# Kernel tuning notes

Hardware: AMD Instinct MI355X
Metric: run time of the kernel (lower is better)

The kernel has to match this reference:

```python
import jax, jax.numpy as jnp
import numpy as np

N_CODES = 1024
DIM = 64
COMMITMENT = 0.25


def setup_inputs() -> dict:
    key = jax.random.key(0)
    k1, k2 = jax.random.split(key)
    z = jax.random.normal(k1, (32, DIM, 64, 64), dtype=jnp.float32)
    # nn.Embedding weight initialized uniform(-1/n_codes, 1/n_codes)
    codebook = jax.random.uniform(
        k2, (N_CODES, DIM), dtype=jnp.float32,
        minval=-1.0 / N_CODES, maxval=1.0 / N_CODES)
    return {"z": z, "codebook": codebook}


def reference(z, codebook):
    B, C, H, W = z.shape
    # (B,C,H,W) -> (B*H*W, C)
    z_flat = jnp.transpose(z, (0, 2, 3, 1)).reshape(-1, C)
    # squared L2 distances via expansion: |z|^2 + |e|^2 - 2 z.e
    dists = (
        jnp.sum(z_flat ** 2, axis=1, keepdims=True)
        + jnp.sum(codebook ** 2, axis=1)
        - 2.0 * z_flat @ codebook.T
    )  # [N, n_codes]
    indices = jnp.argmin(dists, axis=1)  # [N]
    z_q = jnp.transpose(codebook[indices].reshape(B, H, W, C), (0, 3, 1, 2))
    commit_loss = jnp.mean((jax.lax.stop_gradient(z_q) - z) ** 2)
    codebook_loss = jnp.mean((z_q - jax.lax.stop_gradient(z)) ** 2)
    vq_loss = codebook_loss + COMMITMENT * commit_loss
    z_q_st = z + jax.lax.stop_gradient(z_q - z)  # straight-through
    return (z_q_st, vq_loss)
```

## Files before the change

### kernel.cpp

```cpp
#include <hip/hip_runtime.h>


constexpr int DIM    = 64;
constexpr int NCODES = 1024;
constexpr int HWSZ   = 4096;
constexpr int NPOS   = 131072;
constexpr int BLOCK  = 1024;
constexpr int PPB    = 512;
constexpr int GRID   = NPOS / PPB;
constexpr int CIP    = 68;

typedef float    f32x4  __attribute__((ext_vector_type(4)));
typedef int      int4v  __attribute__((ext_vector_type(4)));
typedef unsigned uint4v __attribute__((ext_vector_type(4)));

__global__ __launch_bounds__(BLOCK, 4) void vq_all(const float* __restrict__ z,
                                                   const float* __restrict__ cb,
                                                   float* __restrict__ out) {
    __shared__ __align__(16) unsigned char cb_lds[NCODES * DIM];
    __shared__ int   cinit_lds[16 * CIP];
    __shared__ int   bj_lds[PPB];
    __shared__ float ls_lds[BLOCK / 64];

    const int tid  = threadIdx.x;
    const int w    = tid >> 6;
    const int lane = tid & 63;
    const int q    = lane >> 4;
    const int r    = lane & 15;
    const int p0   = blockIdx.x * PPB;
    const int b    = p0 >> 12;
    const int hwb  = p0 & 4095;

    {
        const int j = tid;
        const float4* src = (const float4*)(cb + (size_t)j * DIM);
        unsigned words[16];
        int nq = 0;
#pragma unroll
        for (int w4 = 0; w4 < 16; w4++) {
            float4 v = src[w4];
            int i0 = __float2int_rn(v.x * 65536.f);
            int i1 = __float2int_rn(v.y * 65536.f);
            int i2 = __float2int_rn(v.z * 65536.f);
            int i3 = __float2int_rn(v.w * 65536.f);
            nq += i0 * i0 + i1 * i1 + i2 * i2 + i3 * i3;
            words[w4] = (unsigned)((i0 & 255) | ((i1 & 255) << 8)
                                 | ((i2 & 255) << 16) | (i3 << 24));
        }
        const int Cj = 262144 - ((nq + 4096) >> 13);
        const int sswz = (j & 3) ^ ((j >> 2) & 1);
#pragma unroll
        for (int u = 0; u < 4; u++) {
            int us = u ^ sswz;
            uint4v tq = {words[4 * u], words[4 * u + 1],
                         words[4 * u + 2], words[4 * u + 3]};
            *(uint4v*)&cb_lds[(size_t)j * 64 + us * 16] = tq;
        }
        cinit_lds[(j & 15) * CIP + (j >> 4)] = (Cj << 10) + (1023 - j);
    }

    int4v afragI[2];
    float zsq[2];
#pragma unroll
    for (int s = 0; s < 2; s++) {
        const float* zb = z + (size_t)b * DIM * HWSZ + hwb + s * 256 + w * 16 + r;
        float sq = 0.f;
        unsigned dw[4];
#pragma unroll
        for (int d = 0; d < 4; d++) {
            float v0 = zb[(size_t)(q * 16 + 4 * d + 0) * HWSZ];
            float v1 = zb[(size_t)(q * 16 + 4 * d + 1) * HWSZ];
            float v2 = zb[(size_t)(q * 16 + 4 * d + 2) * HWSZ];
            float v3 = zb[(size_t)(q * 16 + 4 * d + 3) * HWSZ];
            sq = fmaf(v0, v0, sq); sq = fmaf(v1, v1, sq);
            sq = fmaf(v2, v2, sq); sq = fmaf(v3, v3, sq);
            int i0 = __float2int_rn(v0 * 16.f);
            int i1 = __float2int_rn(v1 * 16.f);
            int i2 = __float2int_rn(v2 * 16.f);
            int i3 = __float2int_rn(v3 * 16.f);
            dw[d] = (unsigned)((i0 & 255) | ((i1 & 255) << 8)
                             | ((i2 & 255) << 16) | (i3 << 24));
        }
        int4v af = {(int)dw[0], (int)dw[1], (int)dw[2], (int)dw[3]};
        afragI[s] = af;
        sq += __shfl_xor(sq, 16, 64);
        sq += __shfl_xor(sq, 32, 64);
        zsq[s] = sq;
    }

    __syncthreads();

    const int bbase = r * 64 + ((q ^ (r & 3) ^ ((r >> 2) & 1)) * 16);

    unsigned best0[4], best1[4], tmp0[4], tmp1[4];
#pragma unroll
    for (int g = 0; g < 4; g++) { best0[g] = 0u; best1[g] = 0u; }

    int4v Bp[4];
    Bp[0] = *(const int4v*)&cb_lds[0 * 1024 + bbase];
    Bp[1] = *(const int4v*)&cb_lds[1 * 1024 + bbase];
    Bp[2] = *(const int4v*)&cb_lds[2 * 1024 + bbase];
    Bp[3] = *(const int4v*)&cb_lds[3 * 1024 + bbase];
    int4v Tq[2];
    Tq[0] = *(const int4v*)&cinit_lds[r * CIP + 0];
    Tq[1] = *(const int4v*)&cinit_lds[r * CIP + 4];
    const int4v cz = {0, 0, 0, 0};

    int4v accR[3][2];

    auto ISSUE = [&](int jt) {
        const int slot = jt & 3;
        int4v B = Bp[slot];
        accR[jt % 3][0] = __builtin_amdgcn_mfma_i32_16x16x64_i8(
            afragI[0], B, cz, 0, 0, 0);
        accR[jt % 3][1] = __builtin_amdgcn_mfma_i32_16x16x64_i8(
            afragI[1], B, cz, 0, 0, 0);
        Bp[slot] = *(const int4v*)&cb_lds[(((jt + 4) & 63) * 1024) + bbase];
    };

    auto PROCESS = [&](int pj) {
        const unsigned Tl = (unsigned)Tq[(pj >> 2) & 1][pj & 3];
#pragma unroll
        for (int g = 0; g < 4; g++) {
            unsigned b0 = ((unsigned)accR[pj % 3][0][g] << 10) + Tl;
            unsigned b1 = ((unsigned)accR[pj % 3][1][g] << 10) + Tl;
            if ((pj & 1) == 0) {
                tmp0[g] = b0; tmp1[g] = b1;
            } else {
                unsigned m0 = tmp0[g] > b0 ? tmp0[g] : b0;
                unsigned m1 = tmp1[g] > b1 ? tmp1[g] : b1;
                best0[g] = best0[g] > m0 ? best0[g] : m0;
                best1[g] = best1[g] > m1 ? best1[g] : m1;
            }
        }
        if ((pj & 3) == 3)
            Tq[(pj >> 2) & 1] =
                *(const int4v*)&cinit_lds[r * CIP + ((((pj >> 2) + 2) & 15) * 4)];
    };

    ISSUE(0);
    ISSUE(1);
#pragma unroll
    for (int jt = 2; jt < 64; jt++) {
        ISSUE(jt);
        PROCESS(jt - 2);
    }
    PROCESS(62);
    PROCESS(63);

    unsigned bestu0[4], bestu1[4];
#pragma unroll
    for (int g = 0; g < 4; g++) {
        unsigned v0 = best0[g];
        unsigned v1 = best1[g];
#pragma unroll
        for (int off = 1; off < 16; off <<= 1) {
            unsigned w0 = (unsigned)__shfl_xor((int)v0, off, 64);
            unsigned w1 = (unsigned)__shfl_xor((int)v1, off, 64);
            v0 = v0 > w0 ? v0 : w0;
            v1 = v1 > w1 ? v1 : w1;
        }
        bestu0[g] = v0; bestu1[g] = v1;
    }

    float lsum = 0.f;
    if (q == (r >> 2)) {
        int g = r & 3;
        unsigned v0 = bestu0[0], v1 = bestu1[0];
        v0 = (g == 1) ? bestu0[1] : v0;  v1 = (g == 1) ? bestu1[1] : v1;
        v0 = (g == 2) ? bestu0[2] : v0;  v1 = (g == 2) ? bestu1[2] : v1;
        v0 = (g == 3) ? bestu0[3] : v0;  v1 = (g == 3) ? bestu1[3] : v1;
        bj_lds[w * 16 + r]       = 1023 - (int)(v0 & 1023u);
        bj_lds[256 + w * 16 + r] = 1023 - (int)(v1 & 1023u);
        lsum = zsq[0] + (float)(262144 - (int)(v0 >> 10)) * (1.f / 524288.f)
             + zsq[1] + (float)(262144 - (int)(v1 >> 10)) * (1.f / 524288.f);
    }
#pragma unroll
    for (int off = 32; off > 0; off >>= 1) lsum += __shfl_down(lsum, off, 64);
    if (lane == 0) ls_lds[w] = lsum;
    __syncthreads();
    if (tid == 0) {
        float s = 0.f;
#pragma unroll
        for (int i = 0; i < BLOCK / 64; i++) s += ls_lds[i];
        atomicAdd(out + (size_t)NPOS * DIM, s * (1.25f / 8388608.f));
    }

    {
        int posi = tid & 511;
        int uu   = tid >> 9;
        int myj  = bj_lds[posi];
        int swzj = (myj & 3) ^ ((myj >> 2) & 1);
        float* ob = out + (size_t)b * DIM * HWSZ + hwb + posi;
#pragma unroll
        for (int k = 0; k < 2; k++) {
            int u  = uu + 2 * k;
            int us = u ^ swzj;
            uint4v t = *(const uint4v*)&cb_lds[(size_t)myj * 64 + us * 16];
#pragma unroll
            for (int wd = 0; wd < 4; wd++) {
                int word = (int)t[wd];
                int cc = u * 16 + wd * 4;
                ob[(size_t)(cc + 0) * HWSZ] =
                    (float)((word << 24) >> 24) * (1.f / 65536.f);
                ob[(size_t)(cc + 1) * HWSZ] =
                    (float)((word << 16) >> 24) * (1.f / 65536.f);
                ob[(size_t)(cc + 2) * HWSZ] =
                    (float)((word << 8) >> 24) * (1.f / 65536.f);
                ob[(size_t)(cc + 3) * HWSZ] =
                    (float)(word >> 24) * (1.f / 65536.f);
            }
        }
    }
}

extern "C" void kernel_launch(void* const* d_in, const int* in_sizes, int n_in,
                              void* d_out, int out_size, void* d_ws, size_t ws_size,
                              hipStream_t stream) {
    const float* z  = (const float*)d_in[0];
    const float* cb = (const float*)d_in[1];
    float* out = (float*)d_out;

    hipMemsetAsync(out + (size_t)NPOS * DIM, 0, sizeof(float), stream);
    vq_all<<<GRID, BLOCK, 0, stream>>>(z, cb, out);
}
```

Baseline: 105.5 us.

## Halve block size and stage codebook in two LDS halves; gather output from global

Blocks shrink to 512 threads covering 256 positions. The quantized codebook is staged in LDS in two 32 KB halves, with a barrier and requantization between them, which cuts LDS per block so more blocks can reside per CU. The output gather now reads the selected fp32 codebook rows from global memory instead of dequantizing the int8 LDS copy, which also makes the output exact. The cost is that each block quantizes the full codebook in two passes with extra barriers, and the grid doubles, so codebook preprocessing is repeated across twice as many blocks.

```diff
diff --git a/kernel.cpp b/kernel.cpp
--- a/kernel.cpp
+++ b/kernel.cpp
@@ -5,9 +5,10 @@
 constexpr int NCODES = 1024;
 constexpr int HWSZ   = 4096;
 constexpr int NPOS   = 131072;
-constexpr int BLOCK  = 1024;
-constexpr int PPB    = 512;
+constexpr int BLOCK  = 512;
+constexpr int PPB    = 256;
 constexpr int GRID   = NPOS / PPB;
+constexpr int HALF   = 512;
 constexpr int CIP    = 68;
 
 typedef float    f32x4  __attribute__((ext_vector_type(4)));
@@ -17,7 +18,7 @@
 __global__ __launch_bounds__(BLOCK, 4) void vq_all(const float* __restrict__ z,
                                                    const float* __restrict__ cb,
                                                    float* __restrict__ out) {
-    __shared__ __align__(16) unsigned char cb_lds[NCODES * DIM];
+    __shared__ __align__(16) unsigned char cb_lds[HALF * DIM];
     __shared__ int   cinit_lds[16 * CIP];
     __shared__ int   bj_lds[PPB];
     __shared__ float ls_lds[BLOCK / 64];
@@ -31,8 +32,8 @@
     const int b    = p0 >> 12;
     const int hwb  = p0 & 4095;
 
-    {
-        const int j = tid;
+    auto QUANT = [&](int h) {
+        const int j = h * HALF + tid;
         const float4* src = (const float4*)(cb + (size_t)j * DIM);
         unsigned words[16];
         int nq = 0;
@@ -54,16 +55,18 @@
             int us = u ^ sswz;
             uint4v tq = {words[4 * u], words[4 * u + 1],
                          words[4 * u + 2], words[4 * u + 3]};
-            *(uint4v*)&cb_lds[(size_t)j * 64 + us * 16] = tq;
+            *(uint4v*)&cb_lds[(size_t)tid * 64 + us * 16] = tq;
         }
         cinit_lds[(j & 15) * CIP + (j >> 4)] = (Cj << 10) + (1023 - j);
-    }
+    };
+
+    QUANT(0);
 
     int4v afragI[2];
     float zsq[2];
 #pragma unroll
     for (int s = 0; s < 2; s++) {
-        const float* zb = z + (size_t)b * DIM * HWSZ + hwb + s * 256 + w * 16 + r;
+        const float* zb = z + (size_t)b * DIM * HWSZ + hwb + w * 32 + s * 16 + r;
         float sq = 0.f;
         unsigned dw[4];
 #pragma unroll
@@ -97,15 +100,8 @@
     for (int g = 0; g < 4; g++) { best0[g] = 0u; best1[g] = 0u; }
 
     int4v Bp[4];
-    Bp[0] = *(const int4v*)&cb_lds[0 * 1024 + bbase];
-    Bp[1] = *(const int4v*)&cb_lds[1 * 1024 + bbase];
-    Bp[2] = *(const int4v*)&cb_lds[2 * 1024 + bbase];
-    Bp[3] = *(const int4v*)&cb_lds[3 * 1024 + bbase];
     int4v Tq[2];
-    Tq[0] = *(const int4v*)&cinit_lds[r * CIP + 0];
-    Tq[1] = *(const int4v*)&cinit_lds[r * CIP + 4];
     const int4v cz = {0, 0, 0, 0};
-
     int4v accR[3][2];
 
     auto ISSUE = [&](int jt) {
@@ -115,7 +111,7 @@
             afragI[0], B, cz, 0, 0, 0);
         accR[jt % 3][1] = __builtin_amdgcn_mfma_i32_16x16x64_i8(
             afragI[1], B, cz, 0, 0, 0);
-        Bp[slot] = *(const int4v*)&cb_lds[(((jt + 4) & 63) * 1024) + bbase];
+        Bp[slot] = *(const int4v*)&cb_lds[(((jt + 4) & 31) * 1024) + bbase];
     };
 
     auto PROCESS = [&](int pj) {
@@ -138,10 +134,38 @@
                 *(const int4v*)&cinit_lds[r * CIP + ((((pj >> 2) + 2) & 15) * 4)];
     };
 
+    Bp[0] = *(const int4v*)&cb_lds[0 * 1024 + bbase];
+    Bp[1] = *(const int4v*)&cb_lds[1 * 1024 + bbase];
+    Bp[2] = *(const int4v*)&cb_lds[2 * 1024 + bbase];
+    Bp[3] = *(const int4v*)&cb_lds[3 * 1024 + bbase];
+    Tq[0] = *(const int4v*)&cinit_lds[r * CIP + 0];
+    Tq[1] = *(const int4v*)&cinit_lds[r * CIP + 4];
+
     ISSUE(0);
     ISSUE(1);
 #pragma unroll
-    for (int jt = 2; jt < 64; jt++) {
+    for (int jt = 2; jt < 32; jt++) {
+        ISSUE(jt);
+        PROCESS(jt - 2);
+    }
+    PROCESS(30);
+    PROCESS(31);
+
+    __syncthreads();
+    QUANT(1);
+    __syncthreads();
+
+    Bp[0] = *(const int4v*)&cb_lds[0 * 1024 + bbase];
+    Bp[1] = *(const int4v*)&cb_lds[1 * 1024 + bbase];
+    Bp[2] = *(const int4v*)&cb_lds[2 * 1024 + bbase];
+    Bp[3] = *(const int4v*)&cb_lds[3 * 1024 + bbase];
+    Tq[0] = *(const int4v*)&cinit_lds[r * CIP + 32];
+    Tq[1] = *(const int4v*)&cinit_lds[r * CIP + 36];
+
+    ISSUE(32);
+    ISSUE(33);
+#pragma unroll
+    for (int jt = 34; jt < 64; jt++) {
         ISSUE(jt);
         PROCESS(jt - 2);
     }
@@ -170,8 +194,8 @@
         v0 = (g == 1) ? bestu0[1] : v0;  v1 = (g == 1) ? bestu1[1] : v1;
         v0 = (g == 2) ? bestu0[2] : v0;  v1 = (g == 2) ? bestu1[2] : v1;
         v0 = (g == 3) ? bestu0[3] : v0;  v1 = (g == 3) ? bestu1[3] : v1;
-        bj_lds[w * 16 + r]       = 1023 - (int)(v0 & 1023u);
-        bj_lds[256 + w * 16 + r] = 1023 - (int)(v1 & 1023u);
+        bj_lds[w * 32 + r]      = 1023 - (int)(v0 & 1023u);
+        bj_lds[w * 32 + 16 + r] = 1023 - (int)(v1 & 1023u);
         lsum = zsq[0] + (float)(262144 - (int)(v0 >> 10)) * (1.f / 524288.f)
              + zsq[1] + (float)(262144 - (int)(v1 >> 10)) * (1.f / 524288.f);
     }
@@ -187,29 +211,31 @@
     }
 
     {
-        int posi = tid & 511;
-        int uu   = tid >> 9;
+        int posi = tid & 255;
+        int uu   = tid >> 8;
         int myj  = bj_lds[posi];
-        int swzj = (myj & 3) ^ ((myj >> 2) & 1);
         float* ob = out + (size_t)b * DIM * HWSZ + hwb + posi;
 #pragma unroll
         for (int k = 0; k < 2; k++) {
-            int u  = uu + 2 * k;
-            int us = u ^ swzj;
-            uint4v t = *(const uint4v*)&cb_lds[(size_t)myj * 64 + us * 16];
-#pragma unroll
-            for (int wd = 0; wd < 4; wd++) {
-                int word = (int)t[wd];
-                int cc = u * 16 + wd * 4;
-                ob[(size_t)(cc + 0) * HWSZ] =
-                    (float)((word << 24) >> 24) * (1.f / 65536.f);
-                ob[(size_t)(cc + 1) * HWSZ] =
-                    (float)((word << 16) >> 24) * (1.f / 65536.f);
-                ob[(size_t)(cc + 2) * HWSZ] =
-                    (float)((word << 8) >> 24) * (1.f / 65536.f);
-                ob[(size_t)(cc + 3) * HWSZ] =
-                    (float)(word >> 24) * (1.f / 65536.f);
-            }
+            int u = uu + 2 * k;
+            const float4* crow = (const float4*)(cb + (size_t)myj * 64 + u * 16);
+            float4 c0 = crow[0], c1 = crow[1], c2 = crow[2], c3 = crow[3];
+            ob[(size_t)(u * 16 +  0) * HWSZ] = c0.x;
+            ob[(size_t)(u * 16 +  1) * HWSZ] = c0.y;
+            ob[(size_t)(u * 16 +  2) * HWSZ] = c0.z;
+            ob[(size_t)(u * 16 +  3) * HWSZ] = c0.w;
+            ob[(size_t)(u * 16 +  4) * HWSZ] = c1.x;
+            ob[(size_t)(u * 16 +  5) * HWSZ] = c1.y;
+            ob[(size_t)(u * 16 +  6) * HWSZ] = c1.z;
+            ob[(size_t)(u * 16 +  7) * HWSZ] = c1.w;
+            ob[(size_t)(u * 16 +  8) * HWSZ] = c2.x;
+            ob[(size_t)(u * 16 +  9) * HWSZ] = c2.y;
+            ob[(size_t)(u * 16 + 10) * HWSZ] = c2.z;
+            ob[(size_t)(u * 16 + 11) * HWSZ] = c2.w;
+            ob[(size_t)(u * 16 + 12) * HWSZ] = c3.x;
+            ob[(size_t)(u * 16 + 13) * HWSZ] = c3.y;
+            ob[(size_t)(u * 16 + 14) * HWSZ] = c3.z;
+            ob[(size_t)(u * 16 + 15) * HWSZ] = c3.w;
         }
     }
 }
```

Result: slower. 112.9 us (+7.1%).
